# Performance work log

Hardware: AMD Instinct MI355X
Metric: run time of the kernel (lower is better)

The kernel has to match this reference:

```python
import jax, jax.numpy as jnp
import numpy as np

B, N_OBJ, N_ATTR = 8, 10000, 2000
IN_DIM, OUT_DIM, ATTR_DIM = 256, 256, 128
E = 800000


def setup_inputs() -> dict:
    key = jax.random.key(0)
    ks = jax.random.split(key, 10)
    object_feats = jax.random.normal(ks[0], (B, N_OBJ, IN_DIM), dtype=jnp.float32)
    attr_feats = jax.random.normal(ks[1], (B, N_ATTR, ATTR_DIM), dtype=jnp.float32)
    src_obj = jax.random.randint(ks[2], (E,), 0, B * N_OBJ)
    src_attr = jax.random.randint(ks[3], (E,), 0, B * N_ATTR)
    edge_index = jnp.stack([src_obj, src_attr], axis=0)  # [2, E]
    edge_weight = jax.random.uniform(ks[4], (E,), dtype=jnp.float32)
    s = 0.02
    W_a2o = jax.random.normal(ks[5], (IN_DIM, ATTR_DIM), dtype=jnp.float32) * s
    b_a2o = jnp.zeros((IN_DIM,), dtype=jnp.float32)
    W_proj = jax.random.normal(ks[6], (OUT_DIM, IN_DIM), dtype=jnp.float32) * s
    b_proj = jnp.zeros((OUT_DIM,), dtype=jnp.float32)
    W_upd = jax.random.normal(ks[7], (OUT_DIM, IN_DIM + OUT_DIM), dtype=jnp.float32) * s
    b_upd = jnp.zeros((OUT_DIM,), dtype=jnp.float32)
    return {
        "object_feats": object_feats,
        "attr_feats": attr_feats,
        "edge_index": edge_index,
        "edge_weight": edge_weight,
        "W_a2o": W_a2o, "b_a2o": b_a2o,
        "W_proj": W_proj, "b_proj": b_proj,
        "W_upd": W_upd, "b_upd": b_upd,
    }


def reference(object_feats, attr_feats, edge_index, edge_weight,
              W_a2o, b_a2o, W_proj, b_proj, W_upd, b_upd):
    bsz, num_objects, in_dim = object_feats.shape
    flat_objects = object_feats.reshape(bsz * num_objects, in_dim)
    flat_attrs = attr_feats.reshape(bsz * attr_feats.shape[1], -1)
    src_obj = edge_index[0]
    src_attr = edge_index[1]
    # gather attr rows, apply linear: [E, in_dim]
    attr_msgs = flat_attrs[src_attr] @ W_a2o.T + b_a2o
    weighted_msgs = attr_msgs * edge_weight[:, None]
    # weighted scatter-add into object slots
    agg = jax.ops.segment_sum(weighted_msgs, src_obj, num_segments=bsz * num_objects)
    weight_sums = jax.ops.segment_sum(edge_weight, src_obj, num_segments=bsz * num_objects)
    agg = agg / jnp.clip(weight_sums, 1e-6)[:, None]
    proj_msgs = agg @ W_proj.T + b_proj
    combined = jnp.concatenate([flat_objects, proj_msgs], axis=-1)
    updated = jax.nn.relu(combined @ W_upd.T + b_upd)  # dropout=0 (eval)
    return updated.reshape(bsz, num_objects, -1)
```

## Files before the change

kernel.cpp:

```cpp
#include <hip/hip_runtime.h>
#include <hip/hip_bf16.h>

#define BSZ      8
#define NOBJ     10000
#define NATTR    2000
#define IN_DIM   256
#define OUT_DIM  256
#define ATTR_DIM 128
#define E_NUM    800000
#define M_ROWS   (BSZ * NOBJ)
#define K_TOT    (IN_DIM + ATTR_DIM)

#define SCAN_CHUNK 1024
#define SCAN_NBLK  ((M_ROWS + SCAN_CHUNK - 1) / SCAN_CHUNK)

typedef short bf16x8 __attribute__((ext_vector_type(8)));
typedef float f32x4  __attribute__((ext_vector_type(4)));

__device__ __forceinline__ short f2bf(float f) {
    union { float f; unsigned u; } v; v.f = f;
    unsigned r = v.u + 0x7FFFu + ((v.u >> 16) & 1u);
    return (short)(r >> 16);
}

__global__ void prep1(const float* __restrict__ W_upd, const float* __restrict__ W_proj,
                      float* __restrict__ M1) {
    int i = blockIdx.x;
    int j = threadIdx.x;
    const float* wrow = W_upd + i * 512 + 256;
    float acc = 0.f;
    for (int k = 0; k < 256; ++k) acc += wrow[k] * W_proj[k * 256 + j];
    M1[i * 256 + j] = acc;
}

__global__ void prep2(const float* __restrict__ W_upd, const float* __restrict__ W_a2o,
                      const float* __restrict__ b_a2o, const float* __restrict__ b_proj,
                      const float* __restrict__ b_upd, const float* __restrict__ M1,
                      unsigned short* __restrict__ Wbig, float* __restrict__ v1,
                      float* __restrict__ v2) {
    int i = blockIdx.x;
    int j = threadIdx.x;
    const float* m1row = M1 + i * 256;
    float acc = 0.f;
    for (int k = 0; k < 256; ++k) acc += m1row[k] * W_a2o[k * 128 + j];
    Wbig[i * K_TOT + 256 + j] = (unsigned short)f2bf(acc);
    Wbig[i * K_TOT + j]       = (unsigned short)f2bf(W_upd[i * 512 + j]);
    Wbig[i * K_TOT + 128 + j] = (unsigned short)f2bf(W_upd[i * 512 + 128 + j]);

    __shared__ float r1[128], r2[128];
    r1[j] = m1row[j] * b_a2o[j] + m1row[j + 128] * b_a2o[j + 128];
    r2[j] = W_upd[i * 512 + 256 + j] * b_proj[j] +
            W_upd[i * 512 + 256 + 128 + j] * b_proj[j + 128];
    __syncthreads();
    for (int s = 64; s > 0; s >>= 1) {
        if (j < s) { r1[j] += r1[j + s]; r2[j] += r2[j + s]; }
        __syncthreads();
    }
    if (j == 0) { v1[i] = r1[0]; v2[i] = r2[0] + b_upd[i]; }
}

__global__ void hist_kernel(const int* __restrict__ ei, int* __restrict__ count) {
    int e = blockIdx.x * blockDim.x + threadIdx.x;
    if (e < E_NUM) atomicAdd(&count[ei[e]], 1);
}

__global__ void scan_partial(const int* __restrict__ count, int* __restrict__ blockSums) {
    __shared__ int sh[256];
    int t = threadIdx.x;
    int base = blockIdx.x * SCAN_CHUNK + t * 4;
    int s = 0;
    if (base + 3 < M_ROWS) {
        int4 v = *reinterpret_cast<const int4*>(count + base);
        s = v.x + v.y + v.z + v.w;
    } else {
        for (int i = 0; i < 4; ++i) if (base + i < M_ROWS) s += count[base + i];
    }
    sh[t] = s;
    __syncthreads();
    for (int off = 128; off > 0; off >>= 1) {
        if (t < off) sh[t] += sh[t + off];
        __syncthreads();
    }
    if (t == 0) blockSums[blockIdx.x] = sh[0];
}

__global__ void scan_sums(const int* __restrict__ blockSums, int* __restrict__ blockOffsets) {
    __shared__ int sh[128];
    int t = threadIdx.x;
    int v = (t < SCAN_NBLK) ? blockSums[t] : 0;
    sh[t] = v;
    __syncthreads();
    for (int off = 1; off < 128; off <<= 1) {
        int u = (t >= off) ? sh[t - off] : 0;
        __syncthreads();
        sh[t] += u;
        __syncthreads();
    }
    if (t < SCAN_NBLK) blockOffsets[t] = sh[t] - v;
}

__global__ void scan_final(const int* __restrict__ count, const int* __restrict__ blockOffsets,
                           int* __restrict__ start, int* __restrict__ cursor) {
    __shared__ int sh[256];
    int t = threadIdx.x;
    int base = blockIdx.x * SCAN_CHUNK + t * 4;
    int c0 = 0, c1 = 0, c2 = 0, c3 = 0;
    if (base + 3 < M_ROWS) {
        int4 v = *reinterpret_cast<const int4*>(count + base);
        c0 = v.x; c1 = v.y; c2 = v.z; c3 = v.w;
    } else {
        if (base + 0 < M_ROWS) c0 = count[base + 0];
        if (base + 1 < M_ROWS) c1 = count[base + 1];
        if (base + 2 < M_ROWS) c2 = count[base + 2];
        if (base + 3 < M_ROWS) c3 = count[base + 3];
    }
    int s = c0 + c1 + c2 + c3;
    sh[t] = s;
    __syncthreads();
    for (int off = 1; off < 256; off <<= 1) {
        int u = (t >= off) ? sh[t - off] : 0;
        __syncthreads();
        sh[t] += u;
        __syncthreads();
    }
    int run = blockOffsets[blockIdx.x] + sh[t] - s;
    if (base + 0 < M_ROWS) { start[base + 0] = run; cursor[base + 0] = run; run += c0; }
    if (base + 1 < M_ROWS) { start[base + 1] = run; cursor[base + 1] = run; run += c1; }
    if (base + 2 < M_ROWS) { start[base + 2] = run; cursor[base + 2] = run; run += c2; }
    if (base + 3 < M_ROWS) { start[base + 3] = run; cursor[base + 3] = run; run += c3; }
    if (blockIdx.x == 0 && t == 0) start[M_ROWS] = E_NUM;
}

__global__ void scatter_kernel(const int* __restrict__ ei, const float* __restrict__ ew,
                               int* __restrict__ cursor, int* __restrict__ s_attr,
                               float* __restrict__ s_w) {
    int e = blockIdx.x * blockDim.x + threadIdx.x;
    if (e < E_NUM) {
        int o = ei[e];
        int pos = atomicAdd(&cursor[o], 1);
        s_attr[pos] = ei[E_NUM + e];
        s_w[pos] = ew[e];
    }
}

__global__ void __launch_bounds__(256) agg_kernel(const float* __restrict__ attrs,
        const int* __restrict__ start, const int* __restrict__ s_attr,
        const float* __restrict__ s_w, float* __restrict__ nrm, float* __restrict__ s_out) {
    int wave = (int)((blockIdx.x * blockDim.x + threadIdx.x) >> 6);
    int lane = threadIdx.x & 63;
    if (wave >= M_ROWS) return;
    int beg = start[wave], end = start[wave + 1];
    float a0 = 0.f, a1 = 0.f, ws = 0.f;
    for (int j = beg; j < end; ++j) {
        int a = s_attr[j];
        float w = s_w[j];
        float2 v = *reinterpret_cast<const float2*>(attrs + (size_t)a * ATTR_DIM + lane * 2);
        a0 += w * v.x; a1 += w * v.y; ws += w;
    }
    float inv = 1.f / fmaxf(ws, 1e-6f);
    float2 o; o.x = a0 * inv; o.y = a1 * inv;
    *reinterpret_cast<float2*>(nrm + (size_t)wave * ATTR_DIM + lane * 2) = o;
    if (lane == 0) s_out[wave] = ws * inv;
}

__global__ void __launch_bounds__(256, 2) gemm_out(
    const float* __restrict__ obj, const float* __restrict__ nrm,
    const unsigned short* __restrict__ Wbig, const float* __restrict__ v1,
    const float* __restrict__ v2, const float* __restrict__ s_arr,
    float* __restrict__ out) {
    __shared__ unsigned short Bs[256][40];

    int tid = threadIdx.x;
    int w = tid >> 6, lane = tid & 63;
    int l15 = lane & 15, quad = lane >> 4;
    int m_base = blockIdx.x * 128 + w * 32;

    f32x4 acc[2][16];
#pragma unroll
    for (int a = 0; a < 2; ++a)
#pragma unroll
        for (int b = 0; b < 16; ++b) acc[a][b] = (f32x4){0.f, 0.f, 0.f, 0.f};

    for (int kt = 0; kt < 12; ++kt) {
        int k0 = kt * 32;
        __syncthreads();
        {
            const int4* src = reinterpret_cast<const int4*>(Wbig + tid * K_TOT + k0);
            int4 q0 = src[0], q1 = src[1], q2 = src[2], q3 = src[3];
            int4* dst = reinterpret_cast<int4*>(&Bs[tid][0]);
            dst[0] = q0; dst[1] = q1; dst[2] = q2; dst[3] = q3;
        }
        __syncthreads();

        bf16x8 af[2];
#pragma unroll
        for (int mt = 0; mt < 2; ++mt) {
            int m = m_base + mt * 16 + l15;
            const float* p;
            if (k0 < 256) p = obj + (size_t)m * 256 + k0 + quad * 8;
            else          p = nrm + (size_t)m * 128 + (k0 - 256) + quad * 8;
            float4 x0 = *reinterpret_cast<const float4*>(p);
            float4 x1 = *reinterpret_cast<const float4*>(p + 4);
            bf16x8 a;
            a[0] = f2bf(x0.x); a[1] = f2bf(x0.y); a[2] = f2bf(x0.z); a[3] = f2bf(x0.w);
            a[4] = f2bf(x1.x); a[5] = f2bf(x1.y); a[6] = f2bf(x1.z); a[7] = f2bf(x1.w);
            af[mt] = a;
        }
#pragma unroll
        for (int nt = 0; nt < 16; ++nt) {
            bf16x8 bf_ = *reinterpret_cast<const bf16x8*>(&Bs[nt * 16 + l15][quad * 8]);
            acc[0][nt] = __builtin_amdgcn_mfma_f32_16x16x32_bf16(af[0], bf_, acc[0][nt], 0, 0, 0);
            acc[1][nt] = __builtin_amdgcn_mfma_f32_16x16x32_bf16(af[1], bf_, acc[1][nt], 0, 0, 0);
        }
    }

    float v1v[16], v2v[16];
#pragma unroll
    for (int nt = 0; nt < 16; ++nt) {
        v1v[nt] = v1[nt * 16 + l15];
        v2v[nt] = v2[nt * 16 + l15];
    }
#pragma unroll
    for (int mt = 0; mt < 2; ++mt) {
#pragma unroll
        for (int r = 0; r < 4; ++r) {
            int m = m_base + mt * 16 + quad * 4 + r;
            float sv = s_arr[m];
            float* orow = out + (size_t)m * 256;
#pragma unroll
            for (int nt = 0; nt < 16; ++nt) {
                float val = acc[mt][nt][r] + sv * v1v[nt] + v2v[nt];
                orow[nt * 16 + l15] = fmaxf(val, 0.f);
            }
        }
    }
}

extern "C" void kernel_launch(void* const* d_in, const int* in_sizes, int n_in,
                              void* d_out, int out_size, void* d_ws, size_t ws_size,
                              hipStream_t stream) {
    const float* obj    = (const float*)d_in[0];
    const float* attrs  = (const float*)d_in[1];
    const int*   ei     = (const int*)d_in[2];
    const float* ew     = (const float*)d_in[3];
    const float* W_a2o  = (const float*)d_in[4];
    const float* b_a2o  = (const float*)d_in[5];
    const float* W_proj = (const float*)d_in[6];
    const float* b_proj = (const float*)d_in[7];
    const float* W_upd  = (const float*)d_in[8];
    const float* b_upd  = (const float*)d_in[9];
    float* out = (float*)d_out;
    char* ws = (char*)d_ws;

    float* nrm            = (float*)(ws);
    float* s_arr          = (float*)(ws + 40960000);
    int*   count          = (int*)  (ws + 41280000);
    int*   start          = (int*)  (ws + 41600000);
    int*   cursor         = (int*)  (ws + 41920256);
    int*   s_attr         = (int*)  (ws + 42240256);
    float* s_w            = (float*)(ws + 45440256);
    float* M1             = (float*)(ws + 48640256);
    unsigned short* Wbig  = (unsigned short*)(ws + 48902400);
    float* v1             = (float*)(ws + 49099008);
    float* v2             = (float*)(ws + 49100032);
    int* blockSums        = (int*)  (ws + 48640256);
    int* blockOffsets     = (int*)  (ws + 48640256 + 512);

    hipMemsetAsync(count, 0, M_ROWS * sizeof(int), stream);

    prep1<<<256, 256, 0, stream>>>(W_upd, W_proj, M1);
    prep2<<<256, 128, 0, stream>>>(W_upd, W_a2o, b_a2o, b_proj, b_upd, M1, Wbig, v1, v2);
    hist_kernel<<<(E_NUM + 255) / 256, 256, 0, stream>>>(ei, count);
    scan_partial<<<SCAN_NBLK, 256, 0, stream>>>(count, blockSums);
    scan_sums<<<1, 128, 0, stream>>>(blockSums, blockOffsets);
    scan_final<<<SCAN_NBLK, 256, 0, stream>>>(count, blockOffsets, start, cursor);
    scatter_kernel<<<(E_NUM + 255) / 256, 256, 0, stream>>>(ei, ew, cursor, s_attr, s_w);
    agg_kernel<<<M_ROWS / 4, 256, 0, stream>>>(attrs, start, s_attr, s_w, nrm, s_arr);
    gemm_out<<<M_ROWS / 128, 256, 0, stream>>>(obj, nrm, Wbig, v1, v2, s_arr, out);
}
```

Baseline: 392.8 us.

## Store attrs and aggregated features in bf16, pack edge records, prefetch edges

Adds a pre-pass that converts attribute features to packed bf16 so the per-edge gather in the aggregation kernel reads half the bytes. Edge attr index and weight are interleaved into one int2 record, and the next record is prefetched inside the loop. The normalized aggregate is written as bf16 and loaded directly as MFMA operands in the GEMM, which removes float-to-bf16 conversion there. Rounding the attributes before the weighted sum adds precision loss compared with rounding only at the GEMM input.

```diff
diff --git a/kernel.cpp b/kernel.cpp
--- a/kernel.cpp
+++ b/kernel.cpp
@@ -21,6 +21,9 @@
     union { float f; unsigned u; } v; v.f = f;
     unsigned r = v.u + 0x7FFFu + ((v.u >> 16) & 1u);
     return (short)(r >> 16);
+}
+__device__ __forceinline__ unsigned pack_bf2(float x, float y) {
+    return ((unsigned)(unsigned short)f2bf(x)) | (((unsigned)(unsigned short)f2bf(y)) << 16);
 }
 
 __global__ void prep1(const float* __restrict__ W_upd, const float* __restrict__ W_proj,
@@ -57,6 +60,12 @@
         __syncthreads();
     }
     if (j == 0) { v1[i] = r1[0]; v2[i] = r2[0] + b_upd[i]; }
+}
+
+__global__ void conv_attrs(const float* __restrict__ attrs, unsigned int* __restrict__ attrs_bf) {
+    int i = blockIdx.x * blockDim.x + threadIdx.x;
+    float2 v = *reinterpret_cast<const float2*>(attrs + (size_t)i * 2);
+    attrs_bf[i] = pack_bf2(v.x, v.y);
 }
 
 __global__ void hist_kernel(const int* __restrict__ ei, int* __restrict__ count) {
@@ -132,39 +141,42 @@
 }
 
 __global__ void scatter_kernel(const int* __restrict__ ei, const float* __restrict__ ew,
-                               int* __restrict__ cursor, int* __restrict__ s_attr,
-                               float* __restrict__ s_w) {
+                               int* __restrict__ cursor, int2* __restrict__ s_edge) {
     int e = blockIdx.x * blockDim.x + threadIdx.x;
     if (e < E_NUM) {
         int o = ei[e];
         int pos = atomicAdd(&cursor[o], 1);
-        s_attr[pos] = ei[E_NUM + e];
-        s_w[pos] = ew[e];
-    }
-}
-
-__global__ void __launch_bounds__(256) agg_kernel(const float* __restrict__ attrs,
-        const int* __restrict__ start, const int* __restrict__ s_attr,
-        const float* __restrict__ s_w, float* __restrict__ nrm, float* __restrict__ s_out) {
+        s_edge[pos] = make_int2(ei[E_NUM + e], __float_as_int(ew[e]));
+    }
+}
+
+__global__ void __launch_bounds__(256) agg_kernel(const unsigned int* __restrict__ attrs_bf,
+        const int* __restrict__ start, const int2* __restrict__ s_edge,
+        unsigned int* __restrict__ nrm, float* __restrict__ s_out) {
     int wave = (int)((blockIdx.x * blockDim.x + threadIdx.x) >> 6);
     int lane = threadIdx.x & 63;
     if (wave >= M_ROWS) return;
     int beg = start[wave], end = start[wave + 1];
     float a0 = 0.f, a1 = 0.f, ws = 0.f;
+    int2 er;
+    if (beg < end) er = s_edge[beg];
     for (int j = beg; j < end; ++j) {
-        int a = s_attr[j];
-        float w = s_w[j];
-        float2 v = *reinterpret_cast<const float2*>(attrs + (size_t)a * ATTR_DIM + lane * 2);
-        a0 += w * v.x; a1 += w * v.y; ws += w;
+        int2 nx;
+        if (j + 1 < end) nx = s_edge[j + 1];
+        float w = __int_as_float(er.y);
+        unsigned int u = attrs_bf[er.x * 64 + lane];
+        a0 += w * __uint_as_float(u << 16);
+        a1 += w * __uint_as_float(u & 0xFFFF0000u);
+        ws += w;
+        er = nx;
     }
     float inv = 1.f / fmaxf(ws, 1e-6f);
-    float2 o; o.x = a0 * inv; o.y = a1 * inv;
-    *reinterpret_cast<float2*>(nrm + (size_t)wave * ATTR_DIM + lane * 2) = o;
+    nrm[wave * 64 + lane] = pack_bf2(a0 * inv, a1 * inv);
     if (lane == 0) s_out[wave] = ws * inv;
 }
 
 __global__ void __launch_bounds__(256, 2) gemm_out(
-    const float* __restrict__ obj, const float* __restrict__ nrm,
+    const float* __restrict__ obj, const unsigned short* __restrict__ nrm,
     const unsigned short* __restrict__ Wbig, const float* __restrict__ v1,
     const float* __restrict__ v2, const float* __restrict__ s_arr,
     float* __restrict__ out) {
@@ -196,15 +208,17 @@
 #pragma unroll
         for (int mt = 0; mt < 2; ++mt) {
             int m = m_base + mt * 16 + l15;
-            const float* p;
-            if (k0 < 256) p = obj + (size_t)m * 256 + k0 + quad * 8;
-            else          p = nrm + (size_t)m * 128 + (k0 - 256) + quad * 8;
-            float4 x0 = *reinterpret_cast<const float4*>(p);
-            float4 x1 = *reinterpret_cast<const float4*>(p + 4);
-            bf16x8 a;
-            a[0] = f2bf(x0.x); a[1] = f2bf(x0.y); a[2] = f2bf(x0.z); a[3] = f2bf(x0.w);
-            a[4] = f2bf(x1.x); a[5] = f2bf(x1.y); a[6] = f2bf(x1.z); a[7] = f2bf(x1.w);
-            af[mt] = a;
+            if (k0 < 256) {
+                const float* p = obj + (size_t)m * 256 + k0 + quad * 8;
+                float4 x0 = *reinterpret_cast<const float4*>(p);
+                float4 x1 = *reinterpret_cast<const float4*>(p + 4);
+                bf16x8 a;
+                a[0] = f2bf(x0.x); a[1] = f2bf(x0.y); a[2] = f2bf(x0.z); a[3] = f2bf(x0.w);
+                a[4] = f2bf(x1.x); a[5] = f2bf(x1.y); a[6] = f2bf(x1.z); a[7] = f2bf(x1.w);
+                af[mt] = a;
+            } else {
+                af[mt] = *reinterpret_cast<const bf16x8*>(nrm + (size_t)m * 128 + (k0 - 256) + quad * 8);
+            }
         }
 #pragma unroll
         for (int nt = 0; nt < 16; ++nt) {
@@ -252,29 +266,30 @@
     float* out = (float*)d_out;
     char* ws = (char*)d_ws;
 
-    float* nrm            = (float*)(ws);
-    float* s_arr          = (float*)(ws + 40960000);
-    int*   count          = (int*)  (ws + 41280000);
-    int*   start          = (int*)  (ws + 41600000);
-    int*   cursor         = (int*)  (ws + 41920256);
-    int*   s_attr         = (int*)  (ws + 42240256);
-    float* s_w            = (float*)(ws + 45440256);
-    float* M1             = (float*)(ws + 48640256);
-    unsigned short* Wbig  = (unsigned short*)(ws + 48902400);
-    float* v1             = (float*)(ws + 49099008);
-    float* v2             = (float*)(ws + 49100032);
-    int* blockSums        = (int*)  (ws + 48640256);
-    int* blockOffsets     = (int*)  (ws + 48640256 + 512);
-
-    hipMemsetAsync(count, 0, M_ROWS * sizeof(int), stream);
+    unsigned int* nrm      = (unsigned int*)(ws);
+    float* s_arr           = (float*)(ws + 20480000);
+    int*   count           = (int*)  (ws + 20800000);
+    int*   start           = (int*)  (ws + 21120000);
+    int*   cursor          = (int*)  (ws + 21440256);
+    int2*  s_edge          = (int2*) (ws + 21760256);
+    unsigned int* attrs_bf = (unsigned int*)(ws + 28160256);
+    float* M1              = (float*)(ws + 32256256);
+    unsigned short* Wbig   = (unsigned short*)(ws + 32518400);
+    float* v1              = (float*)(ws + 32715008);
+    float* v2              = (float*)(ws + 32716032);
+    int* blockSums         = (int*)  (ws + 32256256);
+    int* blockOffsets      = (int*)  (ws + 32256256 + 512);
+
+    (void)hipMemsetAsync(count, 0, M_ROWS * sizeof(int), stream);
 
     prep1<<<256, 256, 0, stream>>>(W_upd, W_proj, M1);
     prep2<<<256, 128, 0, stream>>>(W_upd, W_a2o, b_a2o, b_proj, b_upd, M1, Wbig, v1, v2);
+    conv_attrs<<<(BSZ * NATTR * 64) / 256, 256, 0, stream>>>(attrs, attrs_bf);
     hist_kernel<<<(E_NUM + 255) / 256, 256, 0, stream>>>(ei, count);
     scan_partial<<<SCAN_NBLK, 256, 0, stream>>>(count, blockSums);
     scan_sums<<<1, 128, 0, stream>>>(blockSums, blockOffsets);
     scan_final<<<SCAN_NBLK, 256, 0, stream>>>(count, blockOffsets, start, cursor);
-    scatter_kernel<<<(E_NUM + 255) / 256, 256, 0, stream>>>(ei, ew, cursor, s_attr, s_w);
-    agg_kernel<<<M_ROWS / 4, 256, 0, stream>>>(attrs, start, s_attr, s_w, nrm, s_arr);
-    gemm_out<<<M_ROWS / 128, 256, 0, stream>>>(obj, nrm, Wbig, v1, v2, s_arr, out);
-}
+    scatter_kernel<<<(E_NUM + 255) / 256, 256, 0, stream>>>(ei, ew, cursor, s_edge);
+    agg_kernel<<<M_ROWS / 4, 256, 0, stream>>>(attrs_bf, start, s_edge, nrm, s_arr);
+    gemm_out<<<M_ROWS / 128, 256, 0, stream>>>(obj, (const unsigned short*)nrm, Wbig, v1, v2, s_arr, out);
+}
```

Result: faster. 379.5 us (-3.4%).
